# Performance work log

Measured on AMD Instinct MI355X. Metric: run time of the kernel, lower is better.

Reference implementation:

```python
import jax, jax.numpy as jnp
import numpy as np

B = 16
N = 1024            # num_nodes
U = 64              # num_units
K = 2               # max_diffusion_step
M = K + 1           # num diffusion matrices
F = 2 * U           # inputs + state features per node


def _random_walk(adj):
    # adj: [B, N, N]; faithful to torch: add I, degree = sum over dim 1 (column sums),
    # then diag_embed(d_inv) @ adj (scales rows).
    a = adj + jnp.eye(N, dtype=adj.dtype)
    d = jnp.sum(a, axis=1)                      # [B, N]
    d_inv = jnp.where(d == 0, jnp.zeros_like(d), 1.0 / d)
    return d_inv[:, :, None] * a                # [B, N, N]


def _diffuse(A, x):
    # Faithful reproduction of the torch concat pattern:
    xs = [x]
    if K > 0:
        x1 = jnp.matmul(A, x)
        xs.append(x1)
        for _ in range(2, K + 1):
            x2 = jnp.matmul(A, x1)
            xs.append(x1)
            x1 = x2
    return jnp.stack(xs, axis=-1)               # [B, N, F, M]


def _gconv(inputs, state, A0, A1, W0, b0, W1, b1):
    b = inputs.shape[0]
    x = jnp.concatenate([inputs.reshape(b, N, -1), state.reshape(b, N, -1)], axis=-1)  # [B,N,F]
    f = x.shape[-1]
    x0 = _diffuse(A0, x).reshape(b * N, f * M)
    x1 = _diffuse(A1, x).reshape(b * N, f * M)
    return (x0 @ W0 + b0) + (x1 @ W1 + b1)       # [B*N, out]


def setup_inputs() -> dict:
    key = jax.random.key(0)
    ks = jax.random.split(key, 12)
    din = F * M
    s = 1.0 / np.sqrt(din)
    inputs = jax.random.normal(ks[0], (B, N * U), dtype=jnp.float32)
    hx = jax.random.normal(ks[1], (B, N * U), dtype=jnp.float32)
    adj = jax.random.uniform(ks[2], (B, N, N), dtype=jnp.float32)
    W0 = jax.random.normal(ks[3], (din, 2 * U), dtype=jnp.float32) * s
    b0 = jnp.full((2 * U,), 0.1, dtype=jnp.float32)
    W1 = jax.random.normal(ks[4], (din, 2 * U), dtype=jnp.float32) * s
    b1 = jnp.full((2 * U,), 0.1, dtype=jnp.float32)
    Wc0 = jax.random.normal(ks[5], (din, U), dtype=jnp.float32) * s
    bc0 = jnp.full((U,), 0.1, dtype=jnp.float32)
    Wc1 = jax.random.normal(ks[6], (din, U), dtype=jnp.float32) * s
    bc1 = jnp.full((U,), 0.1, dtype=jnp.float32)
    return {"inputs": inputs, "hx": hx, "adj": adj, "W0": W0, "b0": b0,
            "W1": W1, "b1": b1, "Wc0": Wc0, "bc0": bc0, "Wc1": Wc1, "bc1": bc1}


def reference(inputs, hx, adj, W0, b0, W1, b1, Wc0, bc0, Wc1, bc1):
    b = inputs.shape[0]
    A0 = _random_walk(adj)
    A1 = _random_walk(jnp.transpose(adj, (0, 2, 1)))
    # reset / update gates
    value = jax.nn.sigmoid(_gconv(inputs, hx, A0, A1, W0, b0, W1, b1))  # [B*N, 2U]
    value = value.reshape(b, N, 2 * U)
    r = value[..., :U].reshape(b, N * U)
    u = value[..., U:].reshape(b, N * U)
    # candidate state
    c = _gconv(inputs, r * hx, A0, A1, Wc0, bc0, Wc1, bc1)              # [B*N, U]
    c = jnp.tanh(c).reshape(b, N * U)
    new_state = u * hx + (1.0 - u) * c
    return new_state
```

## Files before the change

kernel.cpp:

```cpp
#include <hip/hip_runtime.h>
#include <hip/hip_bf16.h>

typedef unsigned short u16;
typedef unsigned int u32;
typedef unsigned char u8;
typedef long i64;
typedef __bf16 bf16x8 __attribute__((ext_vector_type(8)));
typedef float floatx4 __attribute__((ext_vector_type(4)));

#define MFMA16(a,b,c) __builtin_amdgcn_mfma_f32_16x16x32_bf16((a),(b),(c),0,0,0)
#define MFMA8(a,b,c)  __builtin_amdgcn_mfma_f32_16x16x32_fp8_fp8((a),(b),(c),0,0,0)
#define AS1 __attribute__((address_space(1)))
#define AS3 __attribute__((address_space(3)))
#define VM6 asm volatile("s_waitcnt vmcnt(6)" ::: "memory")
#define VM4 asm volatile("s_waitcnt vmcnt(4)" ::: "memory")
#define VM3 asm volatile("s_waitcnt vmcnt(3)" ::: "memory")
#define VM2 asm volatile("s_waitcnt vmcnt(2)" ::: "memory")
#define VM0 asm volatile("s_waitcnt vmcnt(0)" ::: "memory")
#define SBAR __builtin_amdgcn_s_barrier()
#define SCHED0 __builtin_amdgcn_sched_barrier(0)

__device__ __forceinline__ void gl16(const void* g, void* l){
  __builtin_amdgcn_global_load_lds((const AS1 void*)g, (AS3 void*)l, 16, 0, 0);
}
__device__ __forceinline__ u16 f2bf(float f){
  u32 u = __builtin_bit_cast(u32, f);
  u += 0x7FFFu + ((u >> 16) & 1u);
  return (u16)(u >> 16);
}
__device__ __forceinline__ float bf2f(u16 h){
  u32 u = ((u32)h) << 16;
  return __builtin_bit_cast(float, u);
}
__device__ __forceinline__ bf16x8 ldfrag(const u16* p){
  return *(const bf16x8*)p;
}
__device__ __forceinline__ u32 pk4(float a, float b, float c, float d){
  int r = __builtin_amdgcn_cvt_pk_fp8_f32(a, b, 0, false);
  r = __builtin_amdgcn_cvt_pk_fp8_f32(c, d, r, true);
  return (u32)r;
}
__device__ __forceinline__ i64 ldA8(const char* chunk, int r, int kf, int lg){
  int sr = r >> 1;
  int G = (((r&1)<<2) + (kf<<1) + (lg>>1)) ^ (sr&7);
  return *(const i64*)(chunk + sr*128 + G*16 + (lg&1)*8);
}

__global__ __launch_bounds__(256) void kp3_prep(
    const float* __restrict__ inp, const float* __restrict__ hx,
    const float* __restrict__ adj,
    const float* __restrict__ W0, const float* __restrict__ b0,
    const float* __restrict__ W1, const float* __restrict__ b1,
    const float* __restrict__ Wc0, const float* __restrict__ bc0,
    const float* __restrict__ Wc1, const float* __restrict__ bc1,
    u16* __restrict__ WgT, u16* __restrict__ WcT,
    float* __restrict__ bias_g, float* __restrict__ bias_c,
    u8* __restrict__ adjf8, u8* __restrict__ adjTf8,
    u8* __restrict__ Xtf8, u16* __restrict__ XC2){
  __shared__ __align__(16) char sh[40960];
  int t = threadIdx.x;
  int blk = blockIdx.x;
  if (blk < 256) {
    float (*XT)[80] = (float(*)[80])sh;
    int r = t >> 2, fq = t & 3;
    int row = blk*64 + r;
    const float4* ip = (const float4*)(inp + (size_t)row*64 + fq*16);
    const float4* hp = (const float4*)(hx  + (size_t)row*64 + fq*16);
    float iv[16], hv[16];
    #pragma unroll
    for (int q=0;q<4;q++){
      float4 a = ip[q]; iv[4*q]=a.x; iv[4*q+1]=a.y; iv[4*q+2]=a.z; iv[4*q+3]=a.w;
      float4 c = hp[q]; hv[4*q]=c.x; hv[4*q+1]=c.y; hv[4*q+2]=c.z; hv[4*q+3]=c.w;
    }
    u32 pi[8];
    #pragma unroll
    for (int q=0;q<8;q++)
      pi[q] = (u32)f2bf(iv[2*q]) | ((u32)f2bf(iv[2*q+1])<<16);
    size_t rbase = (size_t)row*384;
    *(uint4*)(XC2 + rbase + fq*16)     = make_uint4(pi[0],pi[1],pi[2],pi[3]);
    *(uint4*)(XC2 + rbase + fq*16 + 8) = make_uint4(pi[4],pi[5],pi[6],pi[7]);
    #pragma unroll
    for (int q=0;q<16;q++){
      XT[fq*16+q][r]    = iv[q];
      XT[64+fq*16+q][r] = hv[q];
    }
    __syncthreads();
    int feat = t >> 1, half = t & 1;
    int b = blk >> 4, n0 = (blk & 15)*64;
    const float* src = &XT[feat][half*32];
    u32 o[8];
    #pragma unroll
    for (int p=0;p<8;p++)
      o[p] = pk4(src[4*p],src[4*p+1],src[4*p+2],src[4*p+3]);
    u8* dst = Xtf8 + (size_t)b*131072 + (size_t)feat*1024 + n0 + half*32;
    *(uint4*)dst      = make_uint4(o[0],o[1],o[2],o[3]);
    *(uint4*)(dst+16) = make_uint4(o[4],o[5],o[6],o[7]);
    return;
  }
  if (blk < 544) {
    int id = (blk - 256)*256 + t;
    if (id < 128*384) {
      int n = id / 384, k = id % 384;
      float v;
      if (k < 128)       v = W0[(k*3+0)*128 + n] + W1[(k*3+0)*128 + n];
      else if (k < 256){ int f = k-128; v = W0[(f*3+1)*128+n] + W0[(f*3+2)*128+n]; }
      else             { int f = k-256; v = W1[(f*3+1)*128+n] + W1[(f*3+2)*128+n]; }
      WgT[(size_t)n*384 + k] = f2bf(v);
    } else {
      int id2 = id - 128*384;
      int n = id2 / 384, k = id2 % 384;
      float v;
      if (k < 128)       v = Wc0[(k*3+0)*64 + n] + Wc1[(k*3+0)*64 + n];
      else if (k < 256){ int f = k-128; v = Wc0[(f*3+1)*64+n] + Wc0[(f*3+2)*64+n]; }
      else             { int f = k-256; v = Wc1[(f*3+1)*64+n] + Wc1[(f*3+2)*64+n]; }
      WcT[(size_t)n*384 + k] = f2bf(v);
    }
    if (blk == 256) {
      if (t < 128) bias_g[t] = b0[t] + b1[t];
      if (t < 64)  bias_c[t] = bc0[t] + bc1[t];
    }
    return;
  }
  u8* ltb = (u8*)sh;
  int blk2 = blk - 544;
  int b = blk2 >> 7;
  int st = (blk2 >> 3) & 15;
  int h = blk2 & 7;
  int i0 = st*64;
  int r = t >> 2, cq = t & 3;
  size_t base = (size_t)b << 20;
  for (int c = h*2; c < h*2+2; ++c){
    int j0 = c*64, cb = c & 1;
    const float4* s4 = (const float4*)(adj + base + (size_t)(i0 + r)*1024 + j0 + (cq<<4));
    float v[16];
    #pragma unroll
    for (int q = 0; q < 4; q++) {
      float4 f = s4[q];
      v[4*q]=f.x; v[4*q+1]=f.y; v[4*q+2]=f.z; v[4*q+3]=f.w;
    }
    u32 pk[4];
    #pragma unroll
    for (int p = 0; p < 4; p++)
      pk[p] = pk4(v[4*p],v[4*p+1],v[4*p+2],v[4*p+3]);
    *(uint4*)(adjf8 + base + (size_t)(i0 + r)*1024 + j0 + (cq<<4)) =
      make_uint4(pk[0],pk[1],pk[2],pk[3]);
    #pragma unroll
    for (int q = 0; q < 16; q++)
      ltb[cb*4608 + (cq*16+q)*72 + r] = (u8)(pk[q>>2] >> ((q&3)*8));
    __syncthreads();
    u32 w4[4];
    #pragma unroll
    for (int p = 0; p < 4; p++){
      u32 b0v = ltb[cb*4608 + r*72 + cq*16 + 4*p];
      u32 b1v = ltb[cb*4608 + r*72 + cq*16 + 4*p+1];
      u32 b2v = ltb[cb*4608 + r*72 + cq*16 + 4*p+2];
      u32 b3v = ltb[cb*4608 + r*72 + cq*16 + 4*p+3];
      w4[p] = b0v | (b1v<<8) | (b2v<<16) | (b3v<<24);
    }
    *(uint4*)(adjTf8 + base + (size_t)(j0 + r)*1024 + i0 + (cq<<4)) =
      make_uint4(w4[0],w4[1],w4[2],w4[3]);
    __syncthreads();
  }
}

__global__ __launch_bounds__(256) void kg2_gates(
    const u8* __restrict__ adjf8, const u8* __restrict__ adjTf8,
    const u8* __restrict__ Xtf8,
    const float* __restrict__ inp, const float* __restrict__ hx,
    const u16* __restrict__ WgT, const float* __restrict__ bias_g,
    u16* __restrict__ XC2, u8* __restrict__ Stf8, float* __restrict__ uBuf){
  __shared__ __align__(16) char lds[36864];
  int bid = ((blockIdx.x & 7)<<6) + (blockIdx.x >> 3);
  int mt = bid & 31, b = bid >> 5;
  int t = threadIdx.x, w = t>>6, l = t&63, lr = l&15, lg = l>>4;
  int wm = w>>1, wn = w&1;
  int gp = (l&7) ^ ((l>>3)&7);
  size_t off = (size_t)(2*(l>>3) + (gp>>2))*1024 + (gp&3)*16;
  const u8* A0g = adjf8  + ((size_t)b<<20) + (size_t)mt*32768 + off;
  const u8* A1g = adjTf8 + ((size_t)b<<20) + (size_t)mt*32768 + off;
  const u8* Bg  = Xtf8 + (size_t)b*131072 + off;
  floatx4 acc0[4] = {}, acc1[4] = {}, s0 = {}, s1 = {};
  const i64 ONES = 0x3838383838383838L;
  #define STG_KG(bufi, kk) do{ \
    if (w==0){ gl16(A0g+(kk), lds+(bufi)*2048); gl16(A0g+(kk)+16384, lds+(bufi)*2048+1024); gl16(Bg+(kk), lds+12288+(bufi)*8192); } \
    else if (w==1){ gl16(A1g+(kk), lds+6144+(bufi)*2048); gl16(A1g+(kk)+16384, lds+6144+(bufi)*2048+1024); gl16(Bg+(kk)+16384, lds+12288+(bufi)*8192+1024); } \
    else if (w==2){ gl16(Bg+(kk)+32768, lds+12288+(bufi)*8192+2048); gl16(Bg+(kk)+49152, lds+12288+(bufi)*8192+3072); gl16(Bg+(kk)+65536, lds+12288+(bufi)*8192+4096); } \
    else { gl16(Bg+(kk)+81920, lds+12288+(bufi)*8192+5120); gl16(Bg+(kk)+98304, lds+12288+(bufi)*8192+6144); gl16(Bg+(kk)+114688, lds+12288+(bufi)*8192+7168); } \
  }while(0)
  STG_KG(0, 0);
  STG_KG(1, 64);
  int cur = 0;
  for (int step = 0; step < 16; ++step){
    if (step < 14) {
      int nb = cur + 2; if (nb >= 3) nb -= 3;
      STG_KG(nb, (step+2)*64);
      VM6;
    } else if (step == 14) { VM3; } else { VM0; }
    SBAR; SCHED0;
    const char* A0b = lds + cur*2048;
    const char* A1b = lds + 6144 + cur*2048;
    const char* Bb  = lds + 12288 + cur*8192;
    #pragma unroll
    for (int kf=0; kf<2; kf++){
      i64 a0 = ldA8(A0b, wm*16+lr, kf, lg);
      i64 a1 = ldA8(A1b, wm*16+lr, kf, lg);
      s0 = MFMA8(a0, ONES, s0);
      s1 = MFMA8(a1, ONES, s1);
      #pragma unroll
      for (int nf=0; nf<4; nf++){
        i64 bb = ldA8(Bb, wn*64+nf*16+lr, kf, lg);
        acc0[nf] = MFMA8(a0, bb, acc0[nf]);
        acc1[nf] = MFMA8(a1, bb, acc1[nf]);
      }
    }
    SCHED0; SBAR;
    if (++cur == 3) cur = 0;
  }
  __syncthreads();
  u16* SL = (u16*)lds;
  u16* SLT = (u16*)(lds + 25088);
  float d0i[4], d1i[4];
  #pragma unroll
  for (int rr=0; rr<4; rr++){
    d1i[rr] = 1.0f / (s0[rr] + 1.0f);
    d0i[rr] = 1.0f / (s1[rr] + 1.0f);
  }
  #pragma unroll
  for (int nf = 0; nf < 4; nf++) {
    #pragma unroll
    for (int rr = 0; rr < 4; rr++) {
      int rl = wm*16 + lg*4 + rr;
      int row = mt*32 + rl;
      int col = wn*64 + nf*16 + lr;
      float xv = (col < 64) ? inp[(size_t)(b*1024+row)*64 + col]
                            : hx [(size_t)(b*1024+row)*64 + (col-64)];
      float y0 = (acc0[nf][rr] + xv) * d0i[rr];
      float y1 = (acc1[nf][rr] + xv) * d1i[rr];
      u16 b0v = f2bf(y0), b1v = f2bf(y1);
      SL[rl*392 + col]       = f2bf(xv);
      SL[rl*392 + 128 + col] = b0v;
      SL[rl*392 + 256 + col] = b1v;
      if (col < 64) {
        size_t grow = (size_t)(b*1024 + row)*384;
        XC2[grow + 128 + col] = b0v;
        XC2[grow + 256 + col] = b1v;
      }
    }
  }
  __syncthreads();
  floatx4 g[4] = {};
  for (int kk = 0; kk < 384; kk += 32) {
    int ko = kk + lg*8;
    bf16x8 a = ldfrag(&SL[(size_t)(wm*16+lr)*392 + ko]);
    #pragma unroll
    for (int nf = 0; nf < 4; nf++)
      g[nf] = MFMA16(a, ldfrag(WgT + (size_t)(wn*64+nf*16+lr)*384 + ko), g[nf]);
  }
  #pragma unroll
  for (int nf = 0; nf < 4; nf++) {
    #pragma unroll
    for (int rr = 0; rr < 4; rr++) {
      int rl = wm*16 + lg*4 + rr;
      int row = mt*32 + rl;
      int col = wn*64 + nf*16 + lr;
      float pre = g[nf][rr] + bias_g[col];
      float s = 1.0f / (1.0f + __expf(-pre));
      if (col < 64) {
        float shv = s * hx[(size_t)(b*1024+row)*64 + col];
        u16 bv = f2bf(shv);
        XC2[(size_t)(b*1024+row)*384 + 64 + col] = bv;
        SLT[col*40 + rl] = bv;
      } else {
        uBuf[(size_t)(b*1024+row)*64 + (col-64)] = s;
      }
    }
  }
  __syncthreads();
  {
    int c2 = t >> 2, q = t & 3;
    uint4 vv = *(const uint4*)&SLT[c2*40 + q*8];
    u32 arr[4] = {vv.x, vv.y, vv.z, vv.w};
    float f[8];
    #pragma unroll
    for (int e=0;e<8;e++) f[e] = bf2f((u16)(arr[e>>1] >> ((e&1)*16)));
    u32 p0 = pk4(f[0],f[1],f[2],f[3]);
    u32 p1 = pk4(f[4],f[5],f[6],f[7]);
    *(uint2*)(Stf8 + (size_t)b*65536 + (size_t)c2*1024 + mt*32 + q*8) = make_uint2(p0,p1);
  }
  #undef STG_KG
}

__global__ __launch_bounds__(256) void kz2_cand(
    const u8* __restrict__ adjf8, const u8* __restrict__ adjTf8,
    const u8* __restrict__ Stf8,
    const u16* __restrict__ XC2, const u16* __restrict__ WcT,
    const float* __restrict__ bias_c,
    const float* __restrict__ uBuf, const float* __restrict__ hx,
    float* __restrict__ out){
  __shared__ __align__(16) char lds[25088];
  int bid = ((blockIdx.x & 7)<<6) + (blockIdx.x >> 3);
  int mt = bid & 31, b = bid >> 5;
  int t = threadIdx.x, w = t>>6, l = t&63, lr = l&15, lg = l>>4;
  int wm = w>>1, wn = w&1;
  int gp = (l&7) ^ ((l>>3)&7);
  size_t off = (size_t)(2*(l>>3) + (gp>>2))*1024 + (gp&3)*16;
  const u8* A0g = adjf8  + ((size_t)b<<20) + (size_t)mt*32768 + off;
  const u8* A1g = adjTf8 + ((size_t)b<<20) + (size_t)mt*32768 + off;
  const u8* Bg  = Stf8 + (size_t)b*65536 + off;
  floatx4 z0[2] = {}, z1[2] = {}, s0 = {}, s1 = {};
  const i64 ONES = 0x3838383838383838L;
  #define STG_KZ(bufi, kk) do{ \
    if (w==0){ gl16(A0g+(kk), lds+(bufi)*2048); gl16(A0g+(kk)+16384, lds+(bufi)*2048+1024); } \
    else if (w==1){ gl16(A1g+(kk), lds+6144+(bufi)*2048); gl16(A1g+(kk)+16384, lds+6144+(bufi)*2048+1024); } \
    else if (w==2){ gl16(Bg+(kk), lds+12288+(bufi)*4096); gl16(Bg+(kk)+16384, lds+12288+(bufi)*4096+1024); } \
    else { gl16(Bg+(kk)+32768, lds+12288+(bufi)*4096+2048); gl16(Bg+(kk)+49152, lds+12288+(bufi)*4096+3072); } \
  }while(0)
  STG_KZ(0, 0);
  STG_KZ(1, 64);
  int cur = 0;
  for (int step = 0; step < 16; ++step){
    if (step < 14) {
      int nb = cur + 2; if (nb >= 3) nb -= 3;
      STG_KZ(nb, (step+2)*64);
      VM4;
    } else if (step == 14) { VM2; } else { VM0; }
    SBAR; SCHED0;
    const char* A0b = lds + cur*2048;
    const char* A1b = lds + 6144 + cur*2048;
    const char* Bb  = lds + 12288 + cur*4096;
    #pragma unroll
    for (int kf=0; kf<2; kf++){
      i64 a0 = ldA8(A0b, wm*16+lr, kf, lg);
      i64 a1 = ldA8(A1b, wm*16+lr, kf, lg);
      s0 = MFMA8(a0, ONES, s0);
      s1 = MFMA8(a1, ONES, s1);
      #pragma unroll
      for (int nf=0; nf<2; nf++){
        i64 bb = ldA8(Bb, wn*32+nf*16+lr, kf, lg);
        z0[nf] = MFMA8(a0, bb, z0[nf]);
        z1[nf] = MFMA8(a1, bb, z1[nf]);
      }
    }
    SCHED0; SBAR;
    if (++cur == 3) cur = 0;
  }
  __syncthreads();
  u16* SL = (u16*)lds;
  {
    int rl = t >> 3, s = t & 7;
    size_t grow = (size_t)(b*1024 + mt*32 + rl)*384;
    #pragma unroll
    for (int j = 0; j < 3; j++)
      *(uint4*)&SL[(size_t)rl*392 + s*24 + j*8] =
        *(const uint4*)(XC2 + grow + s*24 + j*8);
    *(uint4*)&SL[(size_t)rl*392 + 256 + s*8] =
      *(const uint4*)(XC2 + grow + 256 + s*8);
  }
  float d0i[4], d1i[4];
  #pragma unroll
  for (int rr=0; rr<4; rr++){
    d1i[rr] = 1.0f / (s0[rr] + 1.0f);
    d0i[rr] = 1.0f / (s1[rr] + 1.0f);
  }
  #pragma unroll
  for (int nf = 0; nf < 2; nf++) {
    #pragma unroll
    for (int rr = 0; rr < 4; rr++) {
      int rl = wm*16 + lg*4 + rr;
      int row = mt*32 + rl;
      int col = wn*32 + nf*16 + lr;
      float sval = bf2f(XC2[(size_t)(b*1024+row)*384 + 64 + col]);
      SL[rl*392 + 192 + col] = f2bf((z0[nf][rr] + sval) * d0i[rr]);
      SL[rl*392 + 320 + col] = f2bf((z1[nf][rr] + sval) * d1i[rr]);
    }
  }
  __syncthreads();
  floatx4 c[2] = {};
  for (int kk = 0; kk < 384; kk += 32) {
    int ko = kk + lg*8;
    bf16x8 a = ldfrag(&SL[(size_t)(wm*16+lr)*392 + ko]);
    #pragma unroll
    for (int nf = 0; nf < 2; nf++)
      c[nf] = MFMA16(a, ldfrag(WcT + (size_t)(wn*32+nf*16+lr)*384 + ko), c[nf]);
  }
  #pragma unroll
  for (int nf = 0; nf < 2; nf++) {
    #pragma unroll
    for (int rr = 0; rr < 4; rr++) {
      int row = mt*32 + wm*16 + lg*4 + rr;
      int col = wn*32 + nf*16 + lr;
      float pre = c[nf][rr] + bias_c[col];
      pre = fminf(fmaxf(pre, -15.f), 15.f);
      float e2 = __expf(2.0f*pre);
      float cv = (e2 - 1.0f) / (e2 + 1.0f);
      float u = uBuf[(size_t)(b*1024+row)*64 + col];
      float h = hx[(size_t)(b*1024+row)*64 + col];
      out[(size_t)(b*1024+row)*64 + col] = u*h + (1.0f - u)*cv;
    }
  }
  #undef STG_KZ
}

extern "C" void kernel_launch(void* const* d_in, const int* in_sizes, int n_in,
                              void* d_out, int out_size, void* d_ws, size_t ws_size,
                              hipStream_t stream) {
  (void)in_sizes; (void)n_in; (void)out_size; (void)ws_size;
  const float* inp = (const float*)d_in[0];
  const float* hx  = (const float*)d_in[1];
  const float* adj = (const float*)d_in[2];
  const float* W0  = (const float*)d_in[3];
  const float* b0  = (const float*)d_in[4];
  const float* W1  = (const float*)d_in[5];
  const float* b1  = (const float*)d_in[6];
  const float* Wc0 = (const float*)d_in[7];
  const float* bc0 = (const float*)d_in[8];
  const float* Wc1 = (const float*)d_in[9];
  const float* bc1 = (const float*)d_in[10];
  float* out = (float*)d_out;
  char* ws = (char*)d_ws;

  u8* adjf8   = (u8*)(ws + 0);
  u8* adjTf8  = (u8*)(ws + 16777216);
  u8* Xtf8    = (u8*)(ws + 33554432);
  u16* XC2    = (u16*)(ws + 35651584);
  u8* Stf8    = (u8*)(ws + 48234496);
  float* uBuf = (float*)(ws + 49283072);
  u16* WgT    = (u16*)(ws + 53477376);
  u16* WcT    = (u16*)(ws + 53575680);
  float* bias_g = (float*)(ws + 53624832);
  float* bias_c = (float*)(ws + 53625344);

  hipLaunchKernelGGL(kp3_prep, dim3(2592), dim3(256), 0, stream,
                     inp, hx, adj, W0, b0, W1, b1, Wc0, bc0, Wc1, bc1,
                     WgT, WcT, bias_g, bias_c, adjf8, adjTf8, Xtf8, XC2);
  hipLaunchKernelGGL(kg2_gates, dim3(512), dim3(256), 0, stream,
                     adjf8, adjTf8, Xtf8, inp, hx, WgT, bias_g, XC2, Stf8, uBuf);
  hipLaunchKernelGGL(kz2_cand, dim3(512), dim3(256), 0, stream,
                     adjf8, adjTf8, Stf8, XC2, WcT, bias_c, uBuf, hx, out);
}
```

Measured before the change: 72.30 us.

## Halve row tile to 16, double grid, deepen K-step with double buffering

The gate and candidate kernels now use 16-row tiles instead of 32, doubling the grid to 1024 blocks, with each wave owning a column slice instead of a 2x2 wave split. The K loop now advances 128 per step using two LDS buffers instead of three 64-wide buffers. The prep kernel gives each transpose tile its own block (4640 blocks) instead of looping over two tiles with syncs. This is meant to raise parallelism and occupancy on a 256-CU device, at the cost of each block rereading the full X/S operand for half as many rows, which doubles that operand's traffic.

```diff
diff --git a/kernel.cpp b/kernel.cpp
--- a/kernel.cpp
+++ b/kernel.cpp
@@ -12,10 +12,8 @@
 #define MFMA8(a,b,c)  __builtin_amdgcn_mfma_f32_16x16x32_fp8_fp8((a),(b),(c),0,0,0)
 #define AS1 __attribute__((address_space(1)))
 #define AS3 __attribute__((address_space(3)))
-#define VM6 asm volatile("s_waitcnt vmcnt(6)" ::: "memory")
-#define VM4 asm volatile("s_waitcnt vmcnt(4)" ::: "memory")
+#define VM5 asm volatile("s_waitcnt vmcnt(5)" ::: "memory")
 #define VM3 asm volatile("s_waitcnt vmcnt(3)" ::: "memory")
-#define VM2 asm volatile("s_waitcnt vmcnt(2)" ::: "memory")
 #define VM0 asm volatile("s_waitcnt vmcnt(0)" ::: "memory")
 #define SBAR __builtin_amdgcn_s_barrier()
 #define SCHED0 __builtin_amdgcn_sched_barrier(0)
@@ -123,44 +121,40 @@
   }
   u8* ltb = (u8*)sh;
   int blk2 = blk - 544;
-  int b = blk2 >> 7;
-  int st = (blk2 >> 3) & 15;
-  int h = blk2 & 7;
-  int i0 = st*64;
+  int b = blk2 >> 8;
+  int st = (blk2 >> 4) & 15;
+  int c = blk2 & 15;
+  int i0 = st*64, j0 = c*64;
   int r = t >> 2, cq = t & 3;
   size_t base = (size_t)b << 20;
-  for (int c = h*2; c < h*2+2; ++c){
-    int j0 = c*64, cb = c & 1;
-    const float4* s4 = (const float4*)(adj + base + (size_t)(i0 + r)*1024 + j0 + (cq<<4));
-    float v[16];
-    #pragma unroll
-    for (int q = 0; q < 4; q++) {
-      float4 f = s4[q];
-      v[4*q]=f.x; v[4*q+1]=f.y; v[4*q+2]=f.z; v[4*q+3]=f.w;
-    }
-    u32 pk[4];
-    #pragma unroll
-    for (int p = 0; p < 4; p++)
-      pk[p] = pk4(v[4*p],v[4*p+1],v[4*p+2],v[4*p+3]);
-    *(uint4*)(adjf8 + base + (size_t)(i0 + r)*1024 + j0 + (cq<<4)) =
-      make_uint4(pk[0],pk[1],pk[2],pk[3]);
-    #pragma unroll
-    for (int q = 0; q < 16; q++)
-      ltb[cb*4608 + (cq*16+q)*72 + r] = (u8)(pk[q>>2] >> ((q&3)*8));
-    __syncthreads();
-    u32 w4[4];
-    #pragma unroll
-    for (int p = 0; p < 4; p++){
-      u32 b0v = ltb[cb*4608 + r*72 + cq*16 + 4*p];
-      u32 b1v = ltb[cb*4608 + r*72 + cq*16 + 4*p+1];
-      u32 b2v = ltb[cb*4608 + r*72 + cq*16 + 4*p+2];
-      u32 b3v = ltb[cb*4608 + r*72 + cq*16 + 4*p+3];
-      w4[p] = b0v | (b1v<<8) | (b2v<<16) | (b3v<<24);
-    }
-    *(uint4*)(adjTf8 + base + (size_t)(j0 + r)*1024 + i0 + (cq<<4)) =
-      make_uint4(w4[0],w4[1],w4[2],w4[3]);
-    __syncthreads();
-  }
+  const float4* s4 = (const float4*)(adj + base + (size_t)(i0 + r)*1024 + j0 + (cq<<4));
+  float v[16];
+  #pragma unroll
+  for (int q = 0; q < 4; q++) {
+    float4 f = s4[q];
+    v[4*q]=f.x; v[4*q+1]=f.y; v[4*q+2]=f.z; v[4*q+3]=f.w;
+  }
+  u32 pk[4];
+  #pragma unroll
+  for (int p = 0; p < 4; p++)
+    pk[p] = pk4(v[4*p],v[4*p+1],v[4*p+2],v[4*p+3]);
+  *(uint4*)(adjf8 + base + (size_t)(i0 + r)*1024 + j0 + (cq<<4)) =
+    make_uint4(pk[0],pk[1],pk[2],pk[3]);
+  #pragma unroll
+  for (int q = 0; q < 16; q++)
+    ltb[(cq*16+q)*72 + r] = (u8)(pk[q>>2] >> ((q&3)*8));
+  __syncthreads();
+  u32 w4[4];
+  #pragma unroll
+  for (int p = 0; p < 4; p++){
+    u32 b0v = ltb[r*72 + cq*16 + 4*p];
+    u32 b1v = ltb[r*72 + cq*16 + 4*p+1];
+    u32 b2v = ltb[r*72 + cq*16 + 4*p+2];
+    u32 b3v = ltb[r*72 + cq*16 + 4*p+3];
+    w4[p] = b0v | (b1v<<8) | (b2v<<16) | (b3v<<24);
+  }
+  *(uint4*)(adjTf8 + base + (size_t)(j0 + r)*1024 + i0 + (cq<<4)) =
+    make_uint4(w4[0],w4[1],w4[2],w4[3]);
 }
 
 __global__ __launch_bounds__(256) void kg2_gates(
@@ -169,56 +163,73 @@
     const float* __restrict__ inp, const float* __restrict__ hx,
     const u16* __restrict__ WgT, const float* __restrict__ bias_g,
     u16* __restrict__ XC2, u8* __restrict__ Stf8, float* __restrict__ uBuf){
-  __shared__ __align__(16) char lds[36864];
-  int bid = ((blockIdx.x & 7)<<6) + (blockIdx.x >> 3);
-  int mt = bid & 31, b = bid >> 5;
+  __shared__ __align__(16) char lds[40960];
+  int bid = ((blockIdx.x & 7) << 7) | (blockIdx.x >> 3);
+  int mt = bid & 63, b = bid >> 6;
   int t = threadIdx.x, w = t>>6, l = t&63, lr = l&15, lg = l>>4;
-  int wm = w>>1, wn = w&1;
   int gp = (l&7) ^ ((l>>3)&7);
   size_t off = (size_t)(2*(l>>3) + (gp>>2))*1024 + (gp&3)*16;
-  const u8* A0g = adjf8  + ((size_t)b<<20) + (size_t)mt*32768 + off;
-  const u8* A1g = adjTf8 + ((size_t)b<<20) + (size_t)mt*32768 + off;
+  const u8* A0g = adjf8  + ((size_t)b<<20) + (size_t)mt*16384 + off;
+  const u8* A1g = adjTf8 + ((size_t)b<<20) + (size_t)mt*16384 + off;
   const u8* Bg  = Xtf8 + (size_t)b*131072 + off;
-  floatx4 acc0[4] = {}, acc1[4] = {}, s0 = {}, s1 = {};
+  floatx4 acc0[2] = {}, acc1[2] = {}, s0 = {}, s1 = {};
   const i64 ONES = 0x3838383838383838L;
-  #define STG_KG(bufi, kk) do{ \
-    if (w==0){ gl16(A0g+(kk), lds+(bufi)*2048); gl16(A0g+(kk)+16384, lds+(bufi)*2048+1024); gl16(Bg+(kk), lds+12288+(bufi)*8192); } \
-    else if (w==1){ gl16(A1g+(kk), lds+6144+(bufi)*2048); gl16(A1g+(kk)+16384, lds+6144+(bufi)*2048+1024); gl16(Bg+(kk)+16384, lds+12288+(bufi)*8192+1024); } \
-    else if (w==2){ gl16(Bg+(kk)+32768, lds+12288+(bufi)*8192+2048); gl16(Bg+(kk)+49152, lds+12288+(bufi)*8192+3072); gl16(Bg+(kk)+65536, lds+12288+(bufi)*8192+4096); } \
-    else { gl16(Bg+(kk)+81920, lds+12288+(bufi)*8192+5120); gl16(Bg+(kk)+98304, lds+12288+(bufi)*8192+6144); gl16(Bg+(kk)+114688, lds+12288+(bufi)*8192+7168); } \
+  #define STG_KG(bi, kk) do{ \
+    if (w==0){ \
+      gl16(A0g+(kk),          lds+(bi)*2048); \
+      gl16(A0g+(kk)+64,       lds+(bi)*2048+1024); \
+      gl16(Bg+(kk),           lds+8192+(bi)*16384); \
+      gl16(Bg+(kk)+16384,     lds+8192+(bi)*16384+1024); \
+      gl16(Bg+(kk)+32768,     lds+8192+(bi)*16384+2048); \
+    } else if (w==1){ \
+      gl16(A1g+(kk),          lds+4096+(bi)*2048); \
+      gl16(A1g+(kk)+64,       lds+4096+(bi)*2048+1024); \
+      gl16(Bg+(kk)+49152,     lds+8192+(bi)*16384+3072); \
+      gl16(Bg+(kk)+65536,     lds+8192+(bi)*16384+4096); \
+      gl16(Bg+(kk)+81920,     lds+8192+(bi)*16384+5120); \
+    } else if (w==2){ \
+      gl16(Bg+(kk)+98304,     lds+8192+(bi)*16384+6144); \
+      gl16(Bg+(kk)+114688,    lds+8192+(bi)*16384+7168); \
+      gl16(Bg+(kk)+64,        lds+8192+(bi)*16384+8192); \
+      gl16(Bg+(kk)+64+16384,  lds+8192+(bi)*16384+9216); \
+      gl16(Bg+(kk)+64+32768,  lds+8192+(bi)*16384+10240); \
+    } else { \
+      gl16(Bg+(kk)+64+49152,  lds+8192+(bi)*16384+11264); \
+      gl16(Bg+(kk)+64+65536,  lds+8192+(bi)*16384+12288); \
+      gl16(Bg+(kk)+64+81920,  lds+8192+(bi)*16384+13312); \
+      gl16(Bg+(kk)+64+98304,  lds+8192+(bi)*16384+14336); \
+      gl16(Bg+(kk)+64+114688, lds+8192+(bi)*16384+15360); \
+    } \
   }while(0)
   STG_KG(0, 0);
-  STG_KG(1, 64);
   int cur = 0;
-  for (int step = 0; step < 16; ++step){
-    if (step < 14) {
-      int nb = cur + 2; if (nb >= 3) nb -= 3;
-      STG_KG(nb, (step+2)*64);
-      VM6;
-    } else if (step == 14) { VM3; } else { VM0; }
+  for (int step = 0; step < 8; ++step){
+    if (step < 7) { STG_KG(cur^1, (step+1)*128); VM5; } else { VM0; }
     SBAR; SCHED0;
     const char* A0b = lds + cur*2048;
-    const char* A1b = lds + 6144 + cur*2048;
-    const char* Bb  = lds + 12288 + cur*8192;
-    #pragma unroll
-    for (int kf=0; kf<2; kf++){
-      i64 a0 = ldA8(A0b, wm*16+lr, kf, lg);
-      i64 a1 = ldA8(A1b, wm*16+lr, kf, lg);
+    const char* A1b = lds + 4096 + cur*2048;
+    const char* Bb  = lds + 8192 + cur*16384;
+    #pragma unroll
+    for (int kf=0; kf<4; kf++){
+      int co = kf >> 1, kl = kf & 1;
+      i64 a0 = ldA8(A0b + co*1024, lr, kl, lg);
+      i64 a1 = ldA8(A1b + co*1024, lr, kl, lg);
       s0 = MFMA8(a0, ONES, s0);
       s1 = MFMA8(a1, ONES, s1);
       #pragma unroll
-      for (int nf=0; nf<4; nf++){
-        i64 bb = ldA8(Bb, wn*64+nf*16+lr, kf, lg);
+      for (int nf=0; nf<2; nf++){
+        i64 bb = ldA8(Bb + co*8192, w*32 + nf*16 + lr, kl, lg);
         acc0[nf] = MFMA8(a0, bb, acc0[nf]);
         acc1[nf] = MFMA8(a1, bb, acc1[nf]);
       }
     }
     SCHED0; SBAR;
-    if (++cur == 3) cur = 0;
-  }
+    cur ^= 1;
+  }
+  #undef STG_KG
   __syncthreads();
   u16* SL = (u16*)lds;
-  u16* SLT = (u16*)(lds + 25088);
+  u16* SLT = (u16*)(lds + 12544);
   float d0i[4], d1i[4];
   #pragma unroll
   for (int rr=0; rr<4; rr++){
@@ -226,12 +237,12 @@
     d0i[rr] = 1.0f / (s1[rr] + 1.0f);
   }
   #pragma unroll
-  for (int nf = 0; nf < 4; nf++) {
+  for (int nf = 0; nf < 2; nf++) {
     #pragma unroll
     for (int rr = 0; rr < 4; rr++) {
-      int rl = wm*16 + lg*4 + rr;
-      int row = mt*32 + rl;
-      int col = wn*64 + nf*16 + lr;
+      int rl = lg*4 + rr;
+      int row = mt*16 + rl;
+      int col = w*32 + nf*16 + lr;
       float xv = (col < 64) ? inp[(size_t)(b*1024+row)*64 + col]
                             : hx [(size_t)(b*1024+row)*64 + (col-64)];
       float y0 = (acc0[nf][rr] + xv) * d0i[rr];
@@ -248,28 +259,29 @@
     }
   }
   __syncthreads();
-  floatx4 g[4] = {};
+  floatx4 g[2] = {};
   for (int kk = 0; kk < 384; kk += 32) {
     int ko = kk + lg*8;
-    bf16x8 a = ldfrag(&SL[(size_t)(wm*16+lr)*392 + ko]);
-    #pragma unroll
-    for (int nf = 0; nf < 4; nf++)
-      g[nf] = MFMA16(a, ldfrag(WgT + (size_t)(wn*64+nf*16+lr)*384 + ko), g[nf]);
-  }
-  #pragma unroll
-  for (int nf = 0; nf < 4; nf++) {
+    bf16x8 a = ldfrag(&SL[(size_t)lr*392 + ko]);
+    #pragma unroll
+    for (int nf = 0; nf < 2; nf++)
+      g[nf] = MFMA16(a, ldfrag(WgT + (size_t)(w*32+nf*16+lr)*384 + ko), g[nf]);
+  }
+  __syncthreads();
+  #pragma unroll
+  for (int nf = 0; nf < 2; nf++) {
     #pragma unroll
     for (int rr = 0; rr < 4; rr++) {
-      int rl = wm*16 + lg*4 + rr;
-      int row = mt*32 + rl;
-      int col = wn*64 + nf*16 + lr;
+      int rl = lg*4 + rr;
+      int row = mt*16 + rl;
+      int col = w*32 + nf*16 + lr;
       float pre = g[nf][rr] + bias_g[col];
       float s = 1.0f / (1.0f + __expf(-pre));
       if (col < 64) {
         float shv = s * hx[(size_t)(b*1024+row)*64 + col];
         u16 bv = f2bf(shv);
         XC2[(size_t)(b*1024+row)*384 + 64 + col] = bv;
-        SLT[col*40 + rl] = bv;
+        SLT[col*16 + rl] = bv;
       } else {
         uBuf[(size_t)(b*1024+row)*64 + (col-64)] = s;
       }
@@ -277,17 +289,13 @@
   }
   __syncthreads();
   {
-    int c2 = t >> 2, q = t & 3;
-    uint4 vv = *(const uint4*)&SLT[c2*40 + q*8];
-    u32 arr[4] = {vv.x, vv.y, vv.z, vv.w};
-    float f[8];
-    #pragma unroll
-    for (int e=0;e<8;e++) f[e] = bf2f((u16)(arr[e>>1] >> ((e&1)*16)));
-    u32 p0 = pk4(f[0],f[1],f[2],f[3]);
-    u32 p1 = pk4(f[4],f[5],f[6],f[7]);
-    *(uint2*)(Stf8 + (size_t)b*65536 + (size_t)c2*1024 + mt*32 + q*8) = make_uint2(p0,p1);
-  }
-  #undef STG_KG
+    int feat = t >> 2, q = t & 3;
+    uint2 vv = *(const uint2*)&SLT[feat*16 + q*4];
+    float f0 = bf2f((u16)(vv.x & 0xFFFF)), f1 = bf2f((u16)(vv.x >> 16));
+    float f2 = bf2f((u16)(vv.y & 0xFFFF)), f3 = bf2f((u16)(vv.y >> 16));
+    *(u32*)(Stf8 + (size_t)b*65536 + (size_t)feat*1024 + mt*16 + q*4) =
+      pk4(f0,f1,f2,f3);
+  }
 }
 
 __global__ __launch_bounds__(256) void kz2_cand(
@@ -297,64 +305,69 @@
     const float* __restrict__ bias_c,
     const float* __restrict__ uBuf, const float* __restrict__ hx,
     float* __restrict__ out){
-  __shared__ __align__(16) char lds[25088];
-  int bid = ((blockIdx.x & 7)<<6) + (blockIdx.x >> 3);
-  int mt = bid & 31, b = bid >> 5;
+  __shared__ __align__(16) char lds[24576];
+  int bid = ((blockIdx.x & 7) << 7) | (blockIdx.x >> 3);
+  int mt = bid & 63, b = bid >> 6;
   int t = threadIdx.x, w = t>>6, l = t&63, lr = l&15, lg = l>>4;
-  int wm = w>>1, wn = w&1;
   int gp = (l&7) ^ ((l>>3)&7);
   size_t off = (size_t)(2*(l>>3) + (gp>>2))*1024 + (gp&3)*16;
-  const u8* A0g = adjf8  + ((size_t)b<<20) + (size_t)mt*32768 + off;
-  const u8* A1g = adjTf8 + ((size_t)b<<20) + (size_t)mt*32768 + off;
+  const u8* A0g = adjf8  + ((size_t)b<<20) + (size_t)mt*16384 + off;
+  const u8* A1g = adjTf8 + ((size_t)b<<20) + (size_t)mt*16384 + off;
   const u8* Bg  = Stf8 + (size_t)b*65536 + off;
-  floatx4 z0[2] = {}, z1[2] = {}, s0 = {}, s1 = {};
+  floatx4 z0 = {}, z1 = {}, s0 = {}, s1 = {};
   const i64 ONES = 0x3838383838383838L;
-  #define STG_KZ(bufi, kk) do{ \
-    if (w==0){ gl16(A0g+(kk), lds+(bufi)*2048); gl16(A0g+(kk)+16384, lds+(bufi)*2048+1024); } \
-    else if (w==1){ gl16(A1g+(kk), lds+6144+(bufi)*2048); gl16(A1g+(kk)+16384, lds+6144+(bufi)*2048+1024); } \
-    else if (w==2){ gl16(Bg+(kk), lds+12288+(bufi)*4096); gl16(Bg+(kk)+16384, lds+12288+(bufi)*4096+1024); } \
-    else { gl16(Bg+(kk)+32768, lds+12288+(bufi)*4096+2048); gl16(Bg+(kk)+49152, lds+12288+(bufi)*4096+3072); } \
+  #define STG_KZ(bi, kk) do{ \
+    if (w==0){ \
+      gl16(A0g+(kk),         lds+(bi)*2048); \
+      gl16(A0g+(kk)+64,      lds+(bi)*2048+1024); \
+      gl16(Bg+(kk),          lds+8192+(bi)*8192); \
+    } else if (w==1){ \
+      gl16(A1g+(kk),         lds+4096+(bi)*2048); \
+      gl16(A1g+(kk)+64,      lds+4096+(bi)*2048+1024); \
+      gl16(Bg+(kk)+16384,    lds+8192+(bi)*8192+1024); \
+    } else if (w==2){ \
+      gl16(Bg+(kk)+32768,    lds+8192+(bi)*8192+2048); \
+      gl16(Bg+(kk)+49152,    lds+8192+(bi)*8192+3072); \
+      gl16(Bg+(kk)+64,       lds+8192+(bi)*8192+4096); \
+    } else { \
+      gl16(Bg+(kk)+64+16384, lds+8192+(bi)*8192+5120); \
+      gl16(Bg+(kk)+64+32768, lds+8192+(bi)*8192+6144); \
+      gl16(Bg+(kk)+64+49152, lds+8192+(bi)*8192+7168); \
+    } \
   }while(0)
   STG_KZ(0, 0);
-  STG_KZ(1, 64);
   int cur = 0;
-  for (int step = 0; step < 16; ++step){
-    if (step < 14) {
-      int nb = cur + 2; if (nb >= 3) nb -= 3;
-      STG_KZ(nb, (step+2)*64);
-      VM4;
-    } else if (step == 14) { VM2; } else { VM0; }
+  for (int step = 0; step < 8; ++step){
+    if (step < 7) { STG_KZ(cur^1, (step+1)*128); VM3; } else { VM0; }
     SBAR; SCHED0;
     const char* A0b = lds + cur*2048;
-    const char* A1b = lds + 6144 + cur*2048;
-    const char* Bb  = lds + 12288 + cur*4096;
-    #pragma unroll
-    for (int kf=0; kf<2; kf++){
-      i64 a0 = ldA8(A0b, wm*16+lr, kf, lg);
-      i64 a1 = ldA8(A1b, wm*16+lr, kf, lg);
+    const char* A1b = lds + 4096 + cur*2048;
+    const char* Bb  = lds + 8192 + cur*8192;
+    #pragma unroll
+    for (int kf=0; kf<4; kf++){
+      int co = kf >> 1, kl = kf & 1;
+      i64 a0 = ldA8(A0b + co*1024, lr, kl, lg);
+      i64 a1 = ldA8(A1b + co*1024, lr, kl, lg);
       s0 = MFMA8(a0, ONES, s0);
       s1 = MFMA8(a1, ONES, s1);
-      #pragma unroll
-      for (int nf=0; nf<2; nf++){
-        i64 bb = ldA8(Bb, wn*32+nf*16+lr, kf, lg);
-        z0[nf] = MFMA8(a0, bb, z0[nf]);
-        z1[nf] = MFMA8(a1, bb, z1[nf]);
-      }
+      i64 bb = ldA8(Bb + co*4096, w*16 + lr, kl, lg);
+      z0 = MFMA8(a0, bb, z0);
+      z1 = MFMA8(a1, bb, z1);
     }
     SCHED0; SBAR;
-    if (++cur == 3) cur = 0;
-  }
+    cur ^= 1;
+  }
+  #undef STG_KZ
   __syncthreads();
   u16* SL = (u16*)lds;
   {
-    int rl = t >> 3, s = t & 7;
-    size_t grow = (size_t)(b*1024 + mt*32 + rl)*384;
+    int rl = t >> 4, s = t & 15;
+    size_t grow = (size_t)(b*1024 + mt*16 + rl)*384;
+    size_t base = (size_t)rl*392;
     #pragma unroll
     for (int j = 0; j < 3; j++)
-      *(uint4*)&SL[(size_t)rl*392 + s*24 + j*8] =
-        *(const uint4*)(XC2 + grow + s*24 + j*8);
-    *(uint4*)&SL[(size_t)rl*392 + 256 + s*8] =
-      *(const uint4*)(XC2 + grow + 256 + s*8);
+      *(uint2*)&SL[base + s*12 + j*4] = *(const uint2*)(XC2 + grow + s*12 + j*4);
+    *(uint2*)&SL[base + 256 + s*4] = *(const uint2*)(XC2 + grow + 256 + s*4);
   }
   float d0i[4], d1i[4];
   #pragma unroll
@@ -362,43 +375,34 @@
     d1i[rr] = 1.0f / (s0[rr] + 1.0f);
     d0i[rr] = 1.0f / (s1[rr] + 1.0f);
   }
-  #pragma unroll
-  for (int nf = 0; nf < 2; nf++) {
-    #pragma unroll
-    for (int rr = 0; rr < 4; rr++) {
-      int rl = wm*16 + lg*4 + rr;
-      int row = mt*32 + rl;
-      int col = wn*32 + nf*16 + lr;
-      float sval = bf2f(XC2[(size_t)(b*1024+row)*384 + 64 + col]);
-      SL[rl*392 + 192 + col] = f2bf((z0[nf][rr] + sval) * d0i[rr]);
-      SL[rl*392 + 320 + col] = f2bf((z1[nf][rr] + sval) * d1i[rr]);
-    }
-  }
-  __syncthreads();
-  floatx4 c[2] = {};
+  __syncthreads();
+  #pragma unroll
+  for (int rr = 0; rr < 4; rr++) {
+    int rl = lg*4 + rr;
+    int col = w*16 + lr;
+    float sval = bf2f(SL[rl*392 + 64 + col]);
+    SL[rl*392 + 192 + col] = f2bf((z0[rr] + sval) * d0i[rr]);
+    SL[rl*392 + 320 + col] = f2bf((z1[rr] + sval) * d1i[rr]);
+  }
+  __syncthreads();
+  floatx4 c = {};
   for (int kk = 0; kk < 384; kk += 32) {
     int ko = kk + lg*8;
-    bf16x8 a = ldfrag(&SL[(size_t)(wm*16+lr)*392 + ko]);
-    #pragma unroll
-    for (int nf = 0; nf < 2; nf++)
-      c[nf] = MFMA16(a, ldfrag(WcT + (size_t)(wn*32+nf*16+lr)*384 + ko), c[nf]);
-  }
-  #pragma unroll
-  for (int nf = 0; nf < 2; nf++) {
-    #pragma unroll
-    for (int rr = 0; rr < 4; rr++) {
-      int row = mt*32 + wm*16 + lg*4 + rr;
-      int col = wn*32 + nf*16 + lr;
-      float pre = c[nf][rr] + bias_c[col];
-      pre = fminf(fmaxf(pre, -15.f), 15.f);
-      float e2 = __expf(2.0f*pre);
-      float cv = (e2 - 1.0f) / (e2 + 1.0f);
-      float u = uBuf[(size_t)(b*1024+row)*64 + col];
-      float h = hx[(size_t)(b*1024+row)*64 + col];
-      out[(size_t)(b*1024+row)*64 + col] = u*h + (1.0f - u)*cv;
-    }
-  }
-  #undef STG_KZ
+    bf16x8 a = ldfrag(&SL[(size_t)lr*392 + ko]);
+    c = MFMA16(a, ldfrag(WcT + (size_t)(w*16+lr)*384 + ko), c);
+  }
+  #pragma unroll
+  for (int rr = 0; rr < 4; rr++) {
+    int row = mt*16 + lg*4 + rr;
+    int col = w*16 + lr;
+    float pre = c[rr] + bias_c[col];
+    pre = fminf(fmaxf(pre, -15.f), 15.f);
+    float e2 = __expf(2.0f*pre);
+    float cv = (e2 - 1.0f) / (e2 + 1.0f);
+    float u = uBuf[(size_t)(b*1024+row)*64 + col];
+    float h = hx[(size_t)(b*1024+row)*64 + col];
+    out[(size_t)(b*1024+row)*64 + col] = u*h + (1.0f - u)*cv;
+  }
 }
 
 extern "C" void kernel_launch(void* const* d_in, const int* in_sizes, int n_in,
@@ -430,11 +434,11 @@
   float* bias_g = (float*)(ws + 53624832);
   float* bias_c = (float*)(ws + 53625344);
 
-  hipLaunchKernelGGL(kp3_prep, dim3(2592), dim3(256), 0, stream,
+  hipLaunchKernelGGL(kp3_prep, dim3(4640), dim3(256), 0, stream,
                      inp, hx, adj, W0, b0, W1, b1, Wc0, bc0, Wc1, bc1,
                      WgT, WcT, bias_g, bias_c, adjf8, adjTf8, Xtf8, XC2);
-  hipLaunchKernelGGL(kg2_gates, dim3(512), dim3(256), 0, stream,
+  hipLaunchKernelGGL(kg2_gates, dim3(1024), dim3(256), 0, stream,
                      adjf8, adjTf8, Xtf8, inp, hx, WgT, bias_g, XC2, Stf8, uBuf);
-  hipLaunchKernelGGL(kz2_cand, dim3(512), dim3(256), 0, stream,
+  hipLaunchKernelGGL(kz2_cand, dim3(1024), dim3(256), 0, stream,
                      adjf8, adjTf8, Stf8, XC2, WcT, bias_c, uBuf, hx, out);
 }
```

Result: faster. 64.80 us (median of 2 runs) (-10.4%).
